# Kernel tuning notes

Hardware: AMD Instinct MI355X
Metric: run time of the kernel (lower is better)

## Reference

```python
import jax, jax.numpy as jnp
import numpy as np

DIM = 2048
CTX_DIM = 4096
NUM_HEADS = 16
HEAD_DIM = DIM // NUM_HEADS
EPS = 1e-6


def _rms_norm(x, weight, eps=EPS):
    # RMSNorm over last dim with learned weight (native dtype path for fp32)
    var = jnp.mean(jnp.square(x), axis=-1, keepdims=True)
    return x * jax.lax.rsqrt(var + eps) * weight


def setup_inputs() -> dict:
    key = jax.random.key(0)
    ks = jax.random.split(key, 12)
    B, L, S = 1, 8192, 512
    sd_q = 1.0 / np.sqrt(DIM)
    sd_c = 1.0 / np.sqrt(CTX_DIM)
    return {
        "x": jax.random.normal(ks[0], (B, L, DIM), dtype=jnp.float32),
        "context": jax.random.normal(ks[1], (B, S, CTX_DIM), dtype=jnp.float32),
        "Wq": jax.random.normal(ks[2], (DIM, DIM), dtype=jnp.float32) * sd_q,
        "bq": jax.random.normal(ks[3], (DIM,), dtype=jnp.float32) * 0.01,
        "Wk": jax.random.normal(ks[4], (CTX_DIM, DIM), dtype=jnp.float32) * sd_c,
        "bk": jax.random.normal(ks[5], (DIM,), dtype=jnp.float32) * 0.01,
        "Wv": jax.random.normal(ks[6], (CTX_DIM, DIM), dtype=jnp.float32) * sd_c,
        "bv": jax.random.normal(ks[7], (DIM,), dtype=jnp.float32) * 0.01,
        "Wo": jax.random.normal(ks[8], (DIM, DIM), dtype=jnp.float32) * sd_q,
        "bo": jax.random.normal(ks[9], (DIM,), dtype=jnp.float32) * 0.01,
        "g_q": jnp.ones((DIM,), dtype=jnp.float32),
        "g_k": jnp.ones((DIM,), dtype=jnp.float32),
    }


def reference(x, context, Wq, bq, Wk, bk, Wv, bv, Wo, bo, g_q, g_k):
    B, L, C = x.shape
    S = context.shape[1]
    # QKV projections + RMSNorm on Q,K (over full model dim, pre head split)
    q = _rms_norm(x @ Wq + bq, g_q)           # [B, L, C]
    k = _rms_norm(context @ Wk + bk, g_k)     # [B, S, C]
    v = context @ Wv + bv                     # [B, S, C]
    # split heads
    q = q.reshape(B, L, NUM_HEADS, HEAD_DIM)
    k = k.reshape(B, S, NUM_HEADS, HEAD_DIM)
    v = v.reshape(B, S, NUM_HEADS, HEAD_DIM)
    # non-causal SDPA
    scale = 1.0 / np.sqrt(HEAD_DIM)
    scores = jnp.einsum("blhd,bshd->bhls", q, k) * scale
    probs = jax.nn.softmax(scores, axis=-1)
    attn = jnp.einsum("bhls,bshd->blhd", probs, v).reshape(B, L, C)
    return attn @ Wo + bo
```

## Files before the change

kernel.cpp:

```cpp
#include <hip/hip_runtime.h>
#include <hip/hip_bf16.h>
#include <stdint.h>

#define L_SEQ 8192
#define S_SEQ 512
#define DIM   2048
#define CTX   4096
#define NH    16
#define HD    128

typedef __bf16 bf16_t;
typedef bf16_t bf16x8 __attribute__((ext_vector_type(8)));
typedef float  f32x4_t __attribute__((ext_vector_type(4)));
typedef float  f32x16_t __attribute__((ext_vector_type(16)));

__device__ __forceinline__ ushort f2b(float f) {
  union { float f; uint32_t u; } v; v.f = f;
  uint32_t u = v.u;
  uint32_t r = (u + 0x7fffu + ((u >> 16) & 1u)) >> 16;
  return (ushort)r;
}
__device__ __forceinline__ uint32_t pk2(float a, float b) {
  return (uint32_t)f2b(a) | ((uint32_t)f2b(b) << 16);
}
__device__ __forceinline__ float b2f(ushort u) {
  union { uint32_t u; float f; } v; v.u = ((uint32_t)u) << 16;
  return v.f;
}
__device__ __forceinline__ void gll16(const ushort* g, ushort* l) {
  __builtin_amdgcn_global_load_lds((const __attribute__((address_space(1))) void*)g,
                                   (__attribute__((address_space(3))) void*)l, 16, 0, 0);
}

__global__ __launch_bounds__(256) void k_prep(const float* __restrict__ x,
                                              const float* __restrict__ ctx,
                                              const float* __restrict__ Wq,
                                              const float* __restrict__ Wk,
                                              const float* __restrict__ Wv,
                                              const float* __restrict__ Wo,
                                              const float* __restrict__ gq,
                                              const float* __restrict__ gk,
                                              ushort* __restrict__ xb,
                                              ushort* __restrict__ ctxb,
                                              ushort* __restrict__ wqt,
                                              ushort* __restrict__ wkt,
                                              ushort* __restrict__ wvt,
                                              ushort* __restrict__ wot,
                                              float* __restrict__ g2) {
  const int b = blockIdx.x;
  const int tid = threadIdx.x;
  if (b == 33792) {
    const int d = tid * 8;
#pragma unroll
    for (int j = 0; j < 8; j++) g2[d + j] = gq[d + j] * gk[d + j] * 0.08838834764831843f;
    return;
  }
  if (b < 9216) {
    const float* src; ushort* dst; size_t i;
    if (b < 8192) { src = x;   dst = xb;   i = ((size_t)b * 256 + tid) * 8; }
    else          { src = ctx; dst = ctxb; i = ((size_t)(b - 8192) * 256 + tid) * 8; }
    float4 a = *(const float4*)(src + i);
    float4 c = *(const float4*)(src + i + 4);
    uint4 r;
    r.x = pk2(a.x, a.y); r.y = pk2(a.z, a.w);
    r.z = pk2(c.x, c.y); r.w = pk2(c.z, c.w);
    *(uint4*)(dst + i) = r;
    return;
  }
  __shared__ float t[32][33];
  const float* src; ushort* dst; int K, ti;
  if (b < 13312)      { src = Wq; dst = wqt; K = DIM; ti = b - 9216; }
  else if (b < 21504) { src = Wk; dst = wkt; K = CTX; ti = b - 13312; }
  else if (b < 29696) { src = Wv; dst = wvt; K = CTX; ti = b - 21504; }
  else                { src = Wo; dst = wot; K = DIM; ti = b - 29696; }
  const int n0 = (ti & 63) * 32, k0 = (ti >> 6) * 32;
  const int tx = tid & 31, ty = tid >> 5;
#pragma unroll
  for (int i = 0; i < 4; i++)
    t[ty + 8 * i][tx] = src[(size_t)(k0 + ty + 8 * i) * DIM + n0 + tx];
  __syncthreads();
#pragma unroll
  for (int i = 0; i < 4; i++)
    dst[(size_t)(n0 + ty + 8 * i) * K + k0 + tx] = f2b(t[tx][ty + 8 * i]);
}

__global__ __launch_bounds__(256) void k_qknorm(const ushort* __restrict__ qraw,
                                                const ushort* __restrict__ kraw,
                                                float* __restrict__ qscale,
                                                ushort* __restrict__ kb) {
  const int row = blockIdx.x, tid = threadIdx.x;
  const bool isQ = (row < L_SEQ);
  const ushort* in = isQ ? qraw + (size_t)row * DIM
                         : kraw + (size_t)(row - L_SEQ) * DIM;
  uint4 v = *(const uint4*)(in + tid * 8);
  const uint32_t* vu = (const uint32_t*)&v;
  float f[8];
#pragma unroll
  for (int i = 0; i < 4; i++) {
    f[2 * i]     = b2f((ushort)(vu[i] & 0xffffu));
    f[2 * i + 1] = b2f((ushort)(vu[i] >> 16));
  }
  float s = 0.f;
#pragma unroll
  for (int i = 0; i < 8; i++) s += f[i] * f[i];
#pragma unroll
  for (int off = 32; off; off >>= 1) s += __shfl_down(s, off);
  __shared__ float wsum[4];
  __shared__ float rtot;
  if ((tid & 63) == 0) wsum[tid >> 6] = s;
  __syncthreads();
  if (tid == 0)
    rtot = rsqrtf((wsum[0] + wsum[1] + wsum[2] + wsum[3]) * (1.0f / DIM) + 1e-6f);
  __syncthreads();
  const float rms = rtot;
  if (isQ) {
    if (tid == 0) qscale[row] = rms;
    return;
  }
  ushort r[8];
#pragma unroll
  for (int i = 0; i < 8; i++) r[i] = f2b(f[i] * rms);
  *(uint4*)(kb + (size_t)(row - L_SEQ) * DIM + tid * 8) = *(uint4*)r;
}

template <int OUT_MODE>
__global__ __launch_bounds__(512, 2) void k_gemm256(const ushort* __restrict__ A,
                                                    const ushort* __restrict__ Bt,
                                                    const float* __restrict__ bias,
                                                    void* __restrict__ outp,
                                                    int M, int N, int K) {
  __shared__ __align__(16) ushort lds[65536];
  const int tid = threadIdx.x;
  const int l = tid & 63, wid = tid >> 6;
  const int wm = wid >> 2, wn = wid & 3;
  const int lr = l & 15, lq = l >> 4;

  const int nwg = gridDim.x * gridDim.y;
  const int bid = blockIdx.y * gridDim.x + blockIdx.x;
  const int swz = (bid & 7) * (nwg >> 3) + (bid >> 3);
  const int m0 = (swz / gridDim.x) * 256, n0 = (swz % gridDim.x) * 256;

  f32x4_t acc[8][4];
#pragma unroll
  for (int i = 0; i < 8; i++)
#pragma unroll
    for (int j = 0; j < 4; j++) acc[i][j] = f32x4_t{0.f, 0.f, 0.f, 0.f};

  const int srow = l >> 3;
  const int schunk = ((l & 7) ^ (srow & 7)) * 8;
  auto stage = [&](int buf, int tile, int mat, int h) {
    const ushort* gp = mat ? Bt : A;
    const int rn0 = mat ? n0 : m0;
    const size_t r0 = (size_t)(rn0 + h * 128 + wid * 8 + srow);
    const ushort* g0 = gp + r0 * K + tile * 64 + schunk;
    ushort* l0 = &lds[buf * 32768 + mat * 16384 + (h * 128 + wid * 8) * 64];
    gll16(g0, l0);
    gll16(g0 + (size_t)64 * K, l0 + 64 * 64);
  };

  auto rdA = [&](int buf, int mf, int ks) -> bf16x8 {
    const int R = wm * 128 + mf * 16 + lr;
    return *(const bf16x8*)(&lds[buf * 32768 + R * 64 + (((ks * 4 + lq) ^ (R & 7)) * 8)]);
  };
  auto rdB = [&](int buf, int nf, int ks) -> bf16x8 {
    const int R = wn * 64 + nf * 16 + lr;
    return *(const bf16x8*)(&lds[buf * 32768 + 16384 + R * 64 + (((ks * 4 + lq) ^ (R & 7)) * 8)]);
  };

  const int NT = K >> 6;
  stage(0, 0, 0, 0); stage(0, 0, 0, 1); stage(0, 0, 1, 0); stage(0, 0, 1, 1);

  bf16x8 a[4][2], a2[4][2], b[2][2], b2[2][2];
  for (int kt = 0; kt < NT; kt++) {
    const int cur = kt & 1, nxt = cur ^ 1;
    const bool pf = (kt + 1 < NT);
    if (pf) { stage(nxt, kt + 1, 0, 0); asm volatile("s_waitcnt vmcnt(2)" ::: "memory"); }
    else    { asm volatile("s_waitcnt vmcnt(0)" ::: "memory"); }
    __builtin_amdgcn_sched_barrier(0);
    __builtin_amdgcn_s_barrier();
    __builtin_amdgcn_sched_barrier(0);
#pragma unroll
    for (int mf = 0; mf < 4; mf++) { a[mf][0] = rdA(cur, mf, 0); a[mf][1] = rdA(cur, mf, 1); }
#pragma unroll
    for (int nf = 0; nf < 2; nf++) { b[nf][0] = rdB(cur, nf, 0); b[nf][1] = rdB(cur, nf, 1); }
    __builtin_amdgcn_s_setprio(1);
#pragma unroll
    for (int mf = 0; mf < 4; mf++)
#pragma unroll
      for (int nf = 0; nf < 2; nf++) {
        acc[mf][nf] = __builtin_amdgcn_mfma_f32_16x16x32_bf16(a[mf][0], b[nf][0], acc[mf][nf], 0, 0, 0);
        acc[mf][nf] = __builtin_amdgcn_mfma_f32_16x16x32_bf16(a[mf][1], b[nf][1], acc[mf][nf], 0, 0, 0);
      }
    __builtin_amdgcn_s_setprio(0);
    __builtin_amdgcn_sched_barrier(0);
    __builtin_amdgcn_s_barrier();
    __builtin_amdgcn_sched_barrier(0);
#pragma unroll
    for (int mf = 0; mf < 4; mf++) { a2[mf][0] = rdA(cur, mf + 4, 0); a2[mf][1] = rdA(cur, mf + 4, 1); }
    if (pf) stage(nxt, kt + 1, 0, 1);
    __builtin_amdgcn_sched_barrier(0);
    __builtin_amdgcn_s_barrier();
    __builtin_amdgcn_sched_barrier(0);
    __builtin_amdgcn_s_setprio(1);
#pragma unroll
    for (int mf = 0; mf < 4; mf++)
#pragma unroll
      for (int nf = 0; nf < 2; nf++) {
        acc[mf + 4][nf] = __builtin_amdgcn_mfma_f32_16x16x32_bf16(a2[mf][0], b[nf][0], acc[mf + 4][nf], 0, 0, 0);
        acc[mf + 4][nf] = __builtin_amdgcn_mfma_f32_16x16x32_bf16(a2[mf][1], b[nf][1], acc[mf + 4][nf], 0, 0, 0);
      }
    __builtin_amdgcn_s_setprio(0);
    __builtin_amdgcn_sched_barrier(0);
    __builtin_amdgcn_s_barrier();
    __builtin_amdgcn_sched_barrier(0);
#pragma unroll
    for (int nf = 0; nf < 2; nf++) { b2[nf][0] = rdB(cur, nf + 2, 0); b2[nf][1] = rdB(cur, nf + 2, 1); }
    if (pf) stage(nxt, kt + 1, 1, 0);
    __builtin_amdgcn_sched_barrier(0);
    __builtin_amdgcn_s_barrier();
    __builtin_amdgcn_sched_barrier(0);
    __builtin_amdgcn_s_setprio(1);
#pragma unroll
    for (int mf = 0; mf < 4; mf++)
#pragma unroll
      for (int nf = 0; nf < 2; nf++) {
        acc[mf + 4][nf + 2] = __builtin_amdgcn_mfma_f32_16x16x32_bf16(a2[mf][0], b2[nf][0], acc[mf + 4][nf + 2], 0, 0, 0);
        acc[mf + 4][nf + 2] = __builtin_amdgcn_mfma_f32_16x16x32_bf16(a2[mf][1], b2[nf][1], acc[mf + 4][nf + 2], 0, 0, 0);
      }
    __builtin_amdgcn_s_setprio(0);
    __builtin_amdgcn_sched_barrier(0);
    __builtin_amdgcn_s_barrier();
    __builtin_amdgcn_sched_barrier(0);
#pragma unroll
    for (int mf = 0; mf < 4; mf++) { a[mf][0] = rdA(cur, mf, 0); a[mf][1] = rdA(cur, mf, 1); }
    if (pf) stage(nxt, kt + 1, 1, 1);
    __builtin_amdgcn_sched_barrier(0);
    __builtin_amdgcn_s_barrier();
    __builtin_amdgcn_sched_barrier(0);
    __builtin_amdgcn_s_setprio(1);
#pragma unroll
    for (int mf = 0; mf < 4; mf++)
#pragma unroll
      for (int nf = 0; nf < 2; nf++) {
        acc[mf][nf + 2] = __builtin_amdgcn_mfma_f32_16x16x32_bf16(a[mf][0], b2[nf][0], acc[mf][nf + 2], 0, 0, 0);
        acc[mf][nf + 2] = __builtin_amdgcn_mfma_f32_16x16x32_bf16(a[mf][1], b2[nf][1], acc[mf][nf + 2], 0, 0, 0);
      }
    __builtin_amdgcn_s_setprio(0);
    __builtin_amdgcn_sched_barrier(0);
    __builtin_amdgcn_s_barrier();
    __builtin_amdgcn_sched_barrier(0);
  }

#pragma unroll
  for (int nf = 0; nf < 4; nf++) {
    const int col = n0 + wn * 64 + nf * 16 + lr;
    const float bv = bias[col];
#pragma unroll
    for (int mf = 0; mf < 8; mf++) {
#pragma unroll
      for (int r = 0; r < 4; r++) {
        const int row = m0 + wm * 128 + mf * 16 + lq * 4 + r;
        const float v = acc[mf][nf][r] + bv;
        if constexpr (OUT_MODE == 0)
          ((float*)outp)[(size_t)row * N + col] = v;
        else
          ((ushort*)outp)[(size_t)row * N + col] = f2b(v);
      }
    }
  }
}

__global__ __launch_bounds__(256) void k_gemmkv(const ushort* __restrict__ A,
                                                const ushort* __restrict__ Bt,
                                                const float* __restrict__ biasK,
                                                const float* __restrict__ biasV,
                                                ushort* __restrict__ outK,
                                                ushort* __restrict__ outVt) {
  __shared__ __align__(16) ushort As[4][128 * 32];
  __shared__ __align__(16) ushort Bs[4][64 * 32];
  const int tid = threadIdx.x;
  const int l = tid & 63, wid = tid >> 6;
  const int wr = wid >> 1, wc = wid & 1;
  const int lr = l & 15, lq = l >> 4;
  const int K = CTX, M = S_SEQ;

  const int bid = blockIdx.x;
  const int swz = (bid & 7) * 32 + (bid >> 3);
  const int n0 = (swz >> 2) * 64, m0 = (swz & 3) * 128;

  f32x4_t acc[4][2];
#pragma unroll
  for (int i = 0; i < 4; i++)
#pragma unroll
    for (int j = 0; j < 2; j++) acc[i][j] = f32x4_t{0.f, 0.f, 0.f, 0.f};

  const int srow = l >> 2;
  const int schunk = ((l & 3) ^ ((srow >> 1) & 3)) * 8;
  const ushort* gA = A  + (size_t)(m0 + srow) * K + schunk;
  const ushort* gB = Bt + (size_t)(n0 + wid * 16 + srow) * K + schunk;

  auto stage = [&](int buf, int kt) {
    const int ko = kt * 32;
    gll16(gA + (size_t)(wid * 16) * K + ko,      &As[buf][(wid * 16) * 32]);
    gll16(gA + (size_t)(64 + wid * 16) * K + ko, &As[buf][(64 + wid * 16) * 32]);
    gll16(gB + ko,                               &Bs[buf][(wid * 16) * 32]);
  };
  auto rdA = [&](int buf, int mi) -> bf16x8 {
    const int R = wr * 64 + mi * 16 + lr;
    return *(const bf16x8*)(&As[buf][R * 32 + ((lq ^ ((R >> 1) & 3)) * 8)]);
  };
  auto rdB = [&](int buf, int ni) -> bf16x8 {
    const int R = wc * 32 + ni * 16 + lr;
    return *(const bf16x8*)(&Bs[buf][R * 32 + ((lq ^ ((R >> 1) & 3)) * 8)]);
  };

  const int NT = K >> 5;
  stage(0, 0); stage(1, 1); stage(2, 2);
  for (int t = 0; t < NT; t++) {
    const int cur = t & 3;
    if (t + 3 < NT) { stage((t + 3) & 3, t + 3); asm volatile("s_waitcnt vmcnt(9)" ::: "memory"); }
    else if (t + 2 < NT) { asm volatile("s_waitcnt vmcnt(6)" ::: "memory"); }
    else if (t + 1 < NT) { asm volatile("s_waitcnt vmcnt(3)" ::: "memory"); }
    else                 { asm volatile("s_waitcnt vmcnt(0)" ::: "memory"); }
    __builtin_amdgcn_sched_barrier(0);
    __builtin_amdgcn_s_barrier();
    __builtin_amdgcn_sched_barrier(0);

    bf16x8 af[4], bfr[2];
#pragma unroll
    for (int mi = 0; mi < 4; mi++) af[mi] = rdA(cur, mi);
#pragma unroll
    for (int ni = 0; ni < 2; ni++) bfr[ni] = rdB(cur, ni);
    __builtin_amdgcn_s_setprio(1);
#pragma unroll
    for (int mi = 0; mi < 4; mi++)
#pragma unroll
      for (int ni = 0; ni < 2; ni++)
        acc[mi][ni] = __builtin_amdgcn_mfma_f32_16x16x32_bf16(af[mi], bfr[ni], acc[mi][ni], 0, 0, 0);
    __builtin_amdgcn_s_setprio(0);
    __builtin_amdgcn_sched_barrier(0);
    __builtin_amdgcn_s_barrier();
    __builtin_amdgcn_sched_barrier(0);
  }

#pragma unroll
  for (int mi = 0; mi < 4; mi++) {
#pragma unroll
    for (int ni = 0; ni < 2; ni++) {
      const int col = n0 + wc * 32 + ni * 16 + lr;
      const float bv = (col < DIM) ? biasK[col] : biasV[col - DIM];
#pragma unroll
      for (int r = 0; r < 4; r++) {
        const int row = m0 + wr * 64 + mi * 16 + lq * 4 + r;
        const float v = acc[mi][ni][r] + bv;
        if (col < DIM) outK[(size_t)row * DIM + col] = f2b(v);
        else           outVt[(size_t)(col - DIM) * M + row] = f2b(v);
      }
    }
  }
}

__global__ __launch_bounds__(256) void k_attn(const ushort* __restrict__ Qraw,
                                              const ushort* __restrict__ Kb,
                                              const ushort* __restrict__ Vt,
                                              const float* __restrict__ qscale,
                                              const float* __restrict__ g2,
                                              ushort* __restrict__ Ob) {
  __shared__ __align__(16) ushort smem[16384];
  ushort* Ks = smem;
  ushort* Vs = smem + 64 * 128;

  const int tid = threadIdx.x;
  const int l = tid & 63, wid = tid >> 6;
  const int lo = l & 31, hi = l >> 5;

  const int bid = blockIdx.x;
  const int swz = (bid & 7) * 128 + (bid >> 3);
  const int h = swz >> 6;
  const int q0 = (swz & 63) * 128 + wid * 32;

  bf16x8 qf[8];
  {
    const float qs = qscale[q0 + lo];
    const ushort* qp = Qraw + (size_t)(q0 + lo) * DIM + h * HD + hi * 8;
    const float* gp = g2 + h * HD + hi * 8;
#pragma unroll
    for (int ds = 0; ds < 8; ds++) {
      union { uint4 u; ushort us[8]; } rw;
      rw.u = *(const uint4*)(qp + ds * 16);
      const float* gg = gp + ds * 16;
      union { uint32_t w[4]; bf16x8 v; } ov;
#pragma unroll
      for (int j = 0; j < 4; j++)
        ov.w[j] = pk2(b2f(rw.us[2 * j]) * qs * gg[2 * j],
                      b2f(rw.us[2 * j + 1]) * qs * gg[2 * j + 1]);
      qf[ds] = ov.v;
    }
  }

  f32x16_t o[4] = {};
  float m_run = -1e30f, l_run = 0.f;

  for (int kvb = 0; kvb < S_SEQ / 64; kvb++) {
    __syncthreads();
#pragma unroll
    for (int i = 0; i < 4; i++) {
      const int c = i * 256 + tid, row = c >> 4, cs = c & 15;
      gll16(Kb + (size_t)(kvb * 64 + row) * DIM + h * HD + ((cs ^ (row & 7)) * 8),
            Ks + c * 8);
    }
#pragma unroll
    for (int i = 0; i < 4; i++) {
      const int c = i * 256 + tid, row = c >> 3, cs = c & 7;
      gll16(Vt + (size_t)(h * HD + row) * S_SEQ + kvb * 64 + ((cs ^ (row & 7)) * 8),
            Vs + c * 8);
    }
    __syncthreads();

    f32x16_t sA = {}, sB = {};
#pragma unroll
    for (int ds = 0; ds < 8; ds++) {
      const int ch = ((hi + ds * 2) ^ (lo & 7)) * 8;
      bf16x8 kA = *(const bf16x8*)(Ks + lo * 128 + ch);
      bf16x8 kB = *(const bf16x8*)(Ks + (32 + lo) * 128 + ch);
      sA = __builtin_amdgcn_mfma_f32_32x32x16_bf16(kA, qf[ds], sA, 0, 0, 0);
      sB = __builtin_amdgcn_mfma_f32_32x32x16_bf16(kB, qf[ds], sB, 0, 0, 0);
    }

    float p[32];
#pragma unroll
    for (int i = 0; i < 16; i++) { p[i] = sA[i]; p[16 + i] = sB[i]; }
    float pm = p[0];
#pragma unroll
    for (int i = 1; i < 32; i++) pm = fmaxf(pm, p[i]);
    pm = fmaxf(pm, __shfl_xor(pm, 32));
    const float mn = fmaxf(m_run, pm);
    const float corr = __expf(m_run - mn);
    m_run = mn;
    float ps = 0.f;
#pragma unroll
    for (int i = 0; i < 32; i++) { p[i] = __expf(p[i] - mn); ps += p[i]; }
    ps += __shfl_xor(ps, 32);
    l_run = l_run * corr + ps;
#pragma unroll
    for (int nt = 0; nt < 4; nt++) o[nt] *= corr;

    uint32_t c[16];
#pragma unroll
    for (int j = 0; j < 16; j++) c[j] = pk2(p[2 * j], p[2 * j + 1]);
    bf16x8 pf[4];
#pragma unroll
    for (int s = 0; s < 4; s++) {
      const uint32_t ca = c[4 * s], cb = c[4 * s + 1], cc = c[4 * s + 2], cd = c[4 * s + 3];
      const uint32_t sa = __shfl_xor(ca, 32), sb = __shfl_xor(cb, 32);
      const uint32_t sc = __shfl_xor(cc, 32), sd = __shfl_xor(cd, 32);
      union { uint32_t u[4]; bf16x8 v; } f;
      f.u[0] = hi ? sc : ca; f.u[1] = hi ? sd : cb;
      f.u[2] = hi ? cc : sa; f.u[3] = hi ? cd : sb;
      pf[s] = f.v;
    }

#pragma unroll
    for (int nt = 0; nt < 4; nt++) {
      const int vrow = nt * 32 + lo;
#pragma unroll
      for (int s = 0; s < 4; s++) {
        bf16x8 vf = *(const bf16x8*)(Vs + vrow * 64 + (((s * 2 + hi) ^ (lo & 7)) * 8));
        o[nt] = __builtin_amdgcn_mfma_f32_32x32x16_bf16(vf, pf[s], o[nt], 0, 0, 0);
      }
    }
  }

  const float inv = 1.0f / l_run;
#pragma unroll
  for (int nt = 0; nt < 4; nt++) o[nt] *= inv;

  __syncthreads();
  float* tb = (float*)smem + wid * (32 * 33);
  const int q2 = l >> 1, dh = (l & 1) * 16;
#pragma unroll
  for (int nt = 0; nt < 4; nt++) {
#pragma unroll
    for (int r = 0; r < 16; r++)
      tb[lo * 33 + ((r & 3) + 8 * (r >> 2) + 4 * hi)] = o[nt][r];
    asm volatile("s_waitcnt lgkmcnt(0)" ::: "memory");
    __builtin_amdgcn_sched_barrier(0);
    ushort tmp[16];
#pragma unroll
    for (int j = 0; j < 16; j++) tmp[j] = f2b(tb[q2 * 33 + dh + j]);
    asm volatile("s_waitcnt lgkmcnt(0)" ::: "memory");
    __builtin_amdgcn_sched_barrier(0);
    const size_t oaddr = (size_t)(q0 + q2) * DIM + h * HD + nt * 32 + dh;
    *(uint4*)(Ob + oaddr) = *(uint4*)tmp;
    *(uint4*)(Ob + oaddr + 8) = *(uint4*)(tmp + 8);
  }
}

extern "C" void kernel_launch(void* const* d_in, const int* in_sizes, int n_in,
                              void* d_out, int out_size, void* d_ws, size_t ws_size,
                              hipStream_t stream) {
  const float* x   = (const float*)d_in[0];
  const float* ctx = (const float*)d_in[1];
  const float* Wq  = (const float*)d_in[2];
  const float* bq  = (const float*)d_in[3];
  const float* Wk  = (const float*)d_in[4];
  const float* bk  = (const float*)d_in[5];
  const float* Wv  = (const float*)d_in[6];
  const float* bv  = (const float*)d_in[7];
  const float* Wo  = (const float*)d_in[8];
  const float* bo  = (const float*)d_in[9];
  const float* gq  = (const float*)d_in[10];
  const float* gk  = (const float*)d_in[11];

  char* ws = (char*)d_ws;
  ushort* wqt    = (ushort*)(ws);
  ushort* wkt    = (ushort*)(ws + 8388608);
  ushort* wvt    = (ushort*)(ws + 25165824);
  ushort* wot    = (ushort*)(ws + 41943040);
  ushort* ctxb   = (ushort*)(ws + 50331648);
  float*  qscale = (float*)(ws + 54525952);
  float*  g2     = (float*)(ws + 54558720);
  ushort* kb     = (ushort*)(ws + 83886080);
  ushort* vt     = (ushort*)(ws + 85983232);
  ushort* xb     = (ushort*)(ws + 88080384);
  ushort* kraw   = (ushort*)(ws + 88080384);
  ushort* attnb  = (ushort*)(ws + 88080384);
  ushort* qraw   = (ushort*)(ws + 121634816);

  k_prep<<<33793, 256, 0, stream>>>(x, ctx, Wq, Wk, Wv, Wo, gq, gk,
                                    xb, ctxb, wqt, wkt, wvt, wot, g2);
  k_gemm256<1><<<dim3(DIM / 256, L_SEQ / 256), 512, 0, stream>>>(xb, wqt, bq, qraw, L_SEQ, DIM, DIM);
  k_gemmkv<<<256, 256, 0, stream>>>(ctxb, wkt, bk, bv, kraw, vt);
  k_qknorm<<<L_SEQ + S_SEQ, 256, 0, stream>>>(qraw, kraw, qscale, kb);
  k_attn<<<L_SEQ / 128 * NH, 256, 0, stream>>>(qraw, kb, vt, qscale, g2, attnb);
  k_gemm256<0><<<dim3(DIM / 256, L_SEQ / 256), 512, 0, stream>>>(attnb, wot, bo, d_out, L_SEQ, DIM, DIM);
}
```

Before: 318.9 us.

## Fuse Q RMS sum-of-squares into Q GEMM epilogue and transpose V via LDS

The Q projection GEMM epilogue now computes per-row partial sums of squares into a small partial buffer, and the attention kernel reduces these to get the Q RMS scale. This removes the separate pass that re-read the whole bf16 Q tensor just to compute norms. The K/V GEMM epilogue also stages V through LDS so the transposed V store uses vectorized writes instead of strided scalar stores. Smaller tweaks swap f2b for the native bf16 conversion and use vector loads of g2. The trade-off is extra epilogue work in the Q GEMM and a 32-way partial reduction at the start of each attention wave.

```diff
diff --git a/kernel.cpp b/kernel.cpp
--- a/kernel.cpp
+++ b/kernel.cpp
@@ -15,10 +15,8 @@
 typedef float  f32x16_t __attribute__((ext_vector_type(16)));
 
 __device__ __forceinline__ ushort f2b(float f) {
-  union { float f; uint32_t u; } v; v.f = f;
-  uint32_t u = v.u;
-  uint32_t r = (u + 0x7fffu + ((u >> 16) & 1u)) >> 16;
-  return (ushort)r;
+  bf16_t h = (bf16_t)f;
+  return __builtin_bit_cast(ushort, h);
 }
 __device__ __forceinline__ uint32_t pk2(float a, float b) {
   return (uint32_t)f2b(a) | ((uint32_t)f2b(b) << 16);
@@ -84,15 +82,10 @@
     dst[(size_t)(n0 + ty + 8 * i) * K + k0 + tx] = f2b(t[tx][ty + 8 * i]);
 }
 
-__global__ __launch_bounds__(256) void k_qknorm(const ushort* __restrict__ qraw,
-                                                const ushort* __restrict__ kraw,
-                                                float* __restrict__ qscale,
-                                                ushort* __restrict__ kb) {
+__global__ __launch_bounds__(256) void k_knorm(const ushort* __restrict__ kraw,
+                                               ushort* __restrict__ kb) {
   const int row = blockIdx.x, tid = threadIdx.x;
-  const bool isQ = (row < L_SEQ);
-  const ushort* in = isQ ? qraw + (size_t)row * DIM
-                         : kraw + (size_t)(row - L_SEQ) * DIM;
-  uint4 v = *(const uint4*)(in + tid * 8);
+  uint4 v = *(const uint4*)(kraw + (size_t)row * DIM + tid * 8);
   const uint32_t* vu = (const uint32_t*)&v;
   float f[8];
 #pragma unroll
@@ -113,14 +106,10 @@
     rtot = rsqrtf((wsum[0] + wsum[1] + wsum[2] + wsum[3]) * (1.0f / DIM) + 1e-6f);
   __syncthreads();
   const float rms = rtot;
-  if (isQ) {
-    if (tid == 0) qscale[row] = rms;
-    return;
-  }
   ushort r[8];
 #pragma unroll
   for (int i = 0; i < 8; i++) r[i] = f2b(f[i] * rms);
-  *(uint4*)(kb + (size_t)(row - L_SEQ) * DIM + tid * 8) = *(uint4*)r;
+  *(uint4*)(kb + (size_t)row * DIM + tid * 8) = *(uint4*)r;
 }
 
 template <int OUT_MODE>
@@ -128,6 +117,7 @@
                                                     const ushort* __restrict__ Bt,
                                                     const float* __restrict__ bias,
                                                     void* __restrict__ outp,
+                                                    float* __restrict__ qpart,
                                                     int M, int N, int K) {
   __shared__ __align__(16) ushort lds[65536];
   const int tid = threadIdx.x;
@@ -251,20 +241,41 @@
     __builtin_amdgcn_sched_barrier(0);
   }
 
+  float bvs[4];
+#pragma unroll
+  for (int nf = 0; nf < 4; nf++) bvs[nf] = bias[n0 + wn * 64 + nf * 16 + lr];
 #pragma unroll
   for (int nf = 0; nf < 4; nf++) {
     const int col = n0 + wn * 64 + nf * 16 + lr;
-    const float bv = bias[col];
 #pragma unroll
     for (int mf = 0; mf < 8; mf++) {
 #pragma unroll
       for (int r = 0; r < 4; r++) {
         const int row = m0 + wm * 128 + mf * 16 + lq * 4 + r;
-        const float v = acc[mf][nf][r] + bv;
+        const float v = acc[mf][nf][r] + bvs[nf];
         if constexpr (OUT_MODE == 0)
           ((float*)outp)[(size_t)row * N + col] = v;
         else
           ((ushort*)outp)[(size_t)row * N + col] = f2b(v);
+      }
+    }
+  }
+  if constexpr (OUT_MODE == 1) {
+    const int slot = (n0 >> 8) * 4 + wn;
+#pragma unroll
+    for (int mf = 0; mf < 8; mf++) {
+#pragma unroll
+      for (int r = 0; r < 4; r++) {
+        float s = 0.f;
+#pragma unroll
+        for (int nf = 0; nf < 4; nf++) {
+          const float v = acc[mf][nf][r] + bvs[nf];
+          s += v * v;
+        }
+        s += __shfl_xor(s, 1); s += __shfl_xor(s, 2);
+        s += __shfl_xor(s, 4); s += __shfl_xor(s, 8);
+        if (lr == 0)
+          qpart[(size_t)(m0 + wm * 128 + mf * 16 + lq * 4 + r) * 32 + slot] = s;
       }
     }
   }
@@ -343,27 +354,49 @@
     __builtin_amdgcn_sched_barrier(0);
   }
 
-#pragma unroll
-  for (int mi = 0; mi < 4; mi++) {
-#pragma unroll
-    for (int ni = 0; ni < 2; ni++) {
-      const int col = n0 + wc * 32 + ni * 16 + lr;
-      const float bv = (col < DIM) ? biasK[col] : biasV[col - DIM];
-#pragma unroll
-      for (int r = 0; r < 4; r++) {
-        const int row = m0 + wr * 64 + mi * 16 + lq * 4 + r;
-        const float v = acc[mi][ni][r] + bv;
-        if (col < DIM) outK[(size_t)row * DIM + col] = f2b(v);
-        else           outVt[(size_t)(col - DIM) * M + row] = f2b(v);
-      }
-    }
+  if (n0 < DIM) {
+#pragma unroll
+    for (int mi = 0; mi < 4; mi++) {
+#pragma unroll
+      for (int ni = 0; ni < 2; ni++) {
+        const int col = n0 + wc * 32 + ni * 16 + lr;
+        const float bv = biasK[col];
+#pragma unroll
+        for (int r = 0; r < 4; r++) {
+          const int row = m0 + wr * 64 + mi * 16 + lq * 4 + r;
+          outK[(size_t)row * DIM + col] = f2b(acc[mi][ni][r] + bv);
+        }
+      }
+    }
+  } else {
+    ushort* ldst = &As[0][0];
+    __syncthreads();
+#pragma unroll
+    for (int mi = 0; mi < 4; mi++) {
+#pragma unroll
+      for (int ni = 0; ni < 2; ni++) {
+        const int ccol = wc * 32 + ni * 16 + lr;
+        const float bv = biasV[n0 - DIM + ccol];
+#pragma unroll
+        for (int r = 0; r < 4; r++) {
+          const int crow = wr * 64 + mi * 16 + lq * 4 + r;
+          ldst[ccol * 128 + crow] = f2b(acc[mi][ni][r] + bv);
+        }
+      }
+    }
+    __syncthreads();
+    const int c = tid >> 2, j0 = (tid & 3) * 32;
+    ushort* dst = outVt + (size_t)(n0 - DIM + c) * M + m0 + j0;
+#pragma unroll
+    for (int k2 = 0; k2 < 4; k2++)
+      *(uint4*)(dst + k2 * 8) = *(const uint4*)(ldst + c * 128 + j0 + k2 * 8);
   }
 }
 
 __global__ __launch_bounds__(256) void k_attn(const ushort* __restrict__ Qraw,
                                               const ushort* __restrict__ Kb,
                                               const ushort* __restrict__ Vt,
-                                              const float* __restrict__ qscale,
+                                              const float* __restrict__ qpart,
                                               const float* __restrict__ g2,
                                               ushort* __restrict__ Ob) {
   __shared__ __align__(16) ushort smem[16384];
@@ -381,19 +414,27 @@
 
   bf16x8 qf[8];
   {
-    const float qs = qscale[q0 + lo];
+    float ssum = 0.f;
+    const float* pp = qpart + (size_t)(q0 + lo) * 32;
+#pragma unroll
+    for (int i = 0; i < 8; i++) {
+      float4 t = *(const float4*)(pp + i * 4);
+      ssum += t.x + t.y + t.z + t.w;
+    }
+    const float qs = rsqrtf(ssum * (1.0f / DIM) + 1e-6f);
     const ushort* qp = Qraw + (size_t)(q0 + lo) * DIM + h * HD + hi * 8;
     const float* gp = g2 + h * HD + hi * 8;
 #pragma unroll
     for (int ds = 0; ds < 8; ds++) {
       union { uint4 u; ushort us[8]; } rw;
       rw.u = *(const uint4*)(qp + ds * 16);
-      const float* gg = gp + ds * 16;
+      float4 ga_ = *(const float4*)(gp + ds * 16);
+      float4 gb_ = *(const float4*)(gp + ds * 16 + 4);
       union { uint32_t w[4]; bf16x8 v; } ov;
-#pragma unroll
-      for (int j = 0; j < 4; j++)
-        ov.w[j] = pk2(b2f(rw.us[2 * j]) * qs * gg[2 * j],
-                      b2f(rw.us[2 * j + 1]) * qs * gg[2 * j + 1]);
+      ov.w[0] = pk2(b2f(rw.us[0]) * qs * ga_.x, b2f(rw.us[1]) * qs * ga_.y);
+      ov.w[1] = pk2(b2f(rw.us[2]) * qs * ga_.z, b2f(rw.us[3]) * qs * ga_.w);
+      ov.w[2] = pk2(b2f(rw.us[4]) * qs * gb_.x, b2f(rw.us[5]) * qs * gb_.y);
+      ov.w[3] = pk2(b2f(rw.us[6]) * qs * gb_.z, b2f(rw.us[7]) * qs * gb_.w);
       qf[ds] = ov.v;
     }
   }
@@ -518,8 +559,8 @@
   ushort* wvt    = (ushort*)(ws + 25165824);
   ushort* wot    = (ushort*)(ws + 41943040);
   ushort* ctxb   = (ushort*)(ws + 50331648);
-  float*  qscale = (float*)(ws + 54525952);
   float*  g2     = (float*)(ws + 54558720);
+  float*  qpart  = (float*)(ws + 56623104);
   ushort* kb     = (ushort*)(ws + 83886080);
   ushort* vt     = (ushort*)(ws + 85983232);
   ushort* xb     = (ushort*)(ws + 88080384);
@@ -529,9 +570,9 @@
 
   k_prep<<<33793, 256, 0, stream>>>(x, ctx, Wq, Wk, Wv, Wo, gq, gk,
                                     xb, ctxb, wqt, wkt, wvt, wot, g2);
-  k_gemm256<1><<<dim3(DIM / 256, L_SEQ / 256), 512, 0, stream>>>(xb, wqt, bq, qraw, L_SEQ, DIM, DIM);
+  k_gemm256<1><<<dim3(DIM / 256, L_SEQ / 256), 512, 0, stream>>>(xb, wqt, bq, qraw, qpart, L_SEQ, DIM, DIM);
   k_gemmkv<<<256, 256, 0, stream>>>(ctxb, wkt, bk, bv, kraw, vt);
-  k_qknorm<<<L_SEQ + S_SEQ, 256, 0, stream>>>(qraw, kraw, qscale, kb);
-  k_attn<<<L_SEQ / 128 * NH, 256, 0, stream>>>(qraw, kb, vt, qscale, g2, attnb);
-  k_gemm256<0><<<dim3(DIM / 256, L_SEQ / 256), 512, 0, stream>>>(attnb, wot, bo, d_out, L_SEQ, DIM, DIM);
-}
+  k_knorm<<<S_SEQ, 256, 0, stream>>>(kraw, kb);
+  k_attn<<<L_SEQ / 128 * NH, 256, 0, stream>>>(qraw, kb, vt, qpart, g2, attnb);
+  k_gemm256<0><<<dim3(DIM / 256, L_SEQ / 256), 512, 0, stream>>>(attnb, wot, bo, d_out, nullptr, L_SEQ, DIM, DIM);
+}
```

Measured after the change: 315.3 us. About the same (-1.1%).
